# Performance work log

Measured on AMD Instinct MI355X. Metric: run time of the kernel, lower is better.

## Reference

```python
import jax, jax.numpy as jnp
import numpy as np

B, S1, S2, H, HM = 16, 128, 256, 256, 512  # batch, seq1, seq2, per-token hidden, mlp hidden


def setup_inputs() -> dict:
    k = jax.random.key(0)
    ks = jax.random.split(k, 7)
    query = jax.random.normal(ks[0], (B, S1, H), jnp.float32)
    key = jax.random.normal(ks[1], (B, S2, H), jnp.float32)
    value = jax.random.normal(ks[2], (B, S2, H), jnp.float32)
    q_mask = jax.random.randint(ks[3], (B, S1), 0, 2).astype(jnp.float32)
    k_mask = jax.random.randint(ks[4], (B, S2), 0, 2).astype(jnp.float32)
    s1 = 1.0 / np.sqrt(2 * H)
    W1 = jax.random.uniform(ks[5], (2 * H, HM), jnp.float32, -s1, s1)
    b1 = jnp.zeros((HM,), jnp.float32)
    s2 = 1.0 / np.sqrt(HM)
    W2 = jax.random.uniform(ks[6], (HM, 1), jnp.float32, -s2, s2)
    b2 = jnp.zeros((1,), jnp.float32)
    return {"query": query, "key": key, "value": value, "q_mask": q_mask,
            "k_mask": k_mask, "W1": W1, "b1": b1, "W2": W2, "b2": b2}


def reference(query, key, value, q_mask, k_mask, W1, b1, W2, b2):
    # Factor the first Linear over the concat: cat([q,k]) @ W1 == q @ W1[:H] + k @ W1[H:]
    Hq = query.shape[-1]
    qp = jnp.einsum('bqd,dh->bqh', query, W1[:Hq])      # [B,S1,HM]
    kp = jnp.einsum('bkd,dh->bkh', key, W1[Hq:])        # [B,S2,HM]
    hid = jax.nn.relu(qp[:, :, None, :] + kp[:, None, :, :] + b1)  # [B,S1,S2,HM]
    scores = jnp.einsum('bqkh,h->bqk', hid, W2[:, 0]) + b2[0]       # [B,S1,S2]
    mask = q_mask[:, :, None] * k_mask[:, None, :]                   # [B,S1,S2]
    # masked_fill(-inf).exp() == 0 at masked positions
    A = jnp.where(mask == 0, jnp.zeros((), scores.dtype), jnp.exp(scores))
    A_sum = jnp.clip(jnp.sum(A, axis=-1, keepdims=True), 2e-15, None)
    attn = A / A_sum
    return jnp.einsum('bqk,bkd->bqd', attn, value)  # [B,S1,H]
```

## Files before the change

kernel.cpp:

```cpp
#include <hip/hip_runtime.h>
#include <hip/hip_bf16.h>

#define B_  16
#define S1_ 128
#define S2_ 256
#define H_  256
#define HM_ 512
#define QB  4

typedef _Float16 hf2 __attribute__((ext_vector_type(2)));
typedef _Float16 hf4 __attribute__((ext_vector_type(4)));
typedef _Float16 hf8 __attribute__((ext_vector_type(8)));
typedef float    f32x4 __attribute__((ext_vector_type(4)));

static __device__ inline hf2 u2h(unsigned u) {
    union { unsigned u; hf2 h; } x; x.u = u; return x.h;
}

static __device__ inline float dot2(hf2 a, hf2 b, float c) {
#if __has_builtin(__builtin_amdgcn_fdot2)
    return __builtin_amdgcn_fdot2(a, b, c, false);
#else
    asm("v_dot2_f32_f16 %0, %1, %2, %0" : "+v"(c) : "v"(a), "v"(b));
    return c;
#endif
}

__global__ __launch_bounds__(256) void cvtWB_kernel(
    const float* __restrict__ W1, _Float16* __restrict__ WB)
{
    const int idx  = blockIdx.x * 256 + threadIdx.x;
    const int lane = idx & 63;
    const int nblk = (idx >> 6) & 31;
    const int kblk = idx >> 11;
    const int n    = nblk * 16 + (lane & 15);
    const int k0   = kblk * 32 + (lane >> 4) * 8;
    hf8 v;
#pragma unroll
    for (int j = 0; j < 8; ++j)
        v[j] = (_Float16)W1[(size_t)(k0 + j) * HM_ + n];
    *(hf8*)(WB + (size_t)idx * 8) = v;
}

#define ESTR 520

__global__ __launch_bounds__(512, 4) void proj_mfma_kernel(
    const float* __restrict__ query,
    const float* __restrict__ key,
    const _Float16* __restrict__ WB,
    const float* __restrict__ b1,
    _Float16* __restrict__ QPh,
    _Float16* __restrict__ KPTh)
{
    __shared__ _Float16 Es[16 * ESTR];

    const int t   = threadIdx.x;
    const int bid = blockIdx.x;
    const bool modeK = bid >= 128;
    const int m0  = (modeK ? bid - 128 : bid) * 16;
    const float* X = modeK ? key : query;
    const int kb  = modeK ? 8 : 0;

    {
        const int row = t >> 5, c8 = (t & 31) * 8;
        const float* xs = X + (size_t)(m0 + row) * H_ + c8;
        float4 xa = *(const float4*)xs;
        float4 xb = *(const float4*)(xs + 4);
        hf8 xh = { (_Float16)xa.x, (_Float16)xa.y, (_Float16)xa.z, (_Float16)xa.w,
                   (_Float16)xb.x, (_Float16)xb.y, (_Float16)xb.z, (_Float16)xb.w };
        *(hf8*)&Es[row * ESTR + c8] = xh;
    }
    __syncthreads();

    const int lane = t & 63, w = t >> 6;
    const int fr = lane & 15;
    const int fk = (lane >> 4) * 8;

    f32x4 acc[4] = {};

#pragma unroll
    for (int s = 0; s < 8; ++s) {
        hf8 a = *(const hf8*)&Es[fr * ESTR + s * 32 + fk];
        const _Float16* bp =
            WB + ((((size_t)(kb + s) * 32 + w * 4) * 64) + lane) * 8;
#pragma unroll
        for (int nf = 0; nf < 4; ++nf) {
            hf8 bv = *(const hf8*)(bp + (size_t)nf * 64 * 8);
            acc[nf] = __builtin_amdgcn_mfma_f32_16x16x32_f16(a, bv, acc[nf], 0, 0, 0);
        }
    }

    __syncthreads();

#pragma unroll
    for (int nf = 0; nf < 4; ++nf) {
        const int n = w * 64 + nf * 16 + fr;
        const float bv = modeK ? b1[n] : 0.f;
#pragma unroll
        for (int r = 0; r < 4; ++r) {
            const int ml = (lane >> 4) * 4 + r;
            Es[ml * ESTR + n] = (_Float16)(acc[nf][r] + bv);
        }
    }
    __syncthreads();

    if (!modeK) {
#pragma unroll
        for (int p = 0; p < 2; ++p) {
            const int idx = t + p * 512;
            const int row = idx >> 6, c8 = (idx & 63) * 8;
            *(uint4*)(QPh + (size_t)(m0 + row) * HM_ + c8) =
                *(const uint4*)&Es[row * ESTR + c8];
        }
    } else {
        const int bb = m0 >> 8, kbase = m0 & 255;
#pragma unroll
        for (int p = 0; p < 2; ++p) {
            const int idx = t + p * 512;
            const int h8 = idx >> 4, kl = idx & 15;
            *(uint4*)(KPTh + (((size_t)bb * 64 + h8) * 256 + kbase + kl) * 8) =
                *(const uint4*)&Es[kl * ESTR + h8 * 8];
        }
    }
}

__global__ __launch_bounds__(512, 4) void attn_kernel(
    const _Float16* __restrict__ QPh,
    const _Float16* __restrict__ KPTh,
    const float* __restrict__ value,
    const float* __restrict__ q_mask,
    const float* __restrict__ k_mask,
    const float* __restrict__ W2,
    const float* __restrict__ b2,
    float* __restrict__ out)
{
    __shared__ __align__(16) _Float16 qp_h[QB][HM_];
    __shared__ __align__(16) _Float16 w2_h[HM_];
    __shared__ __align__(16) float    Ap[2][QB][S2_];
    __shared__ __align__(16) float4   opart[8][QB][64];
    __shared__ float rA_s[QB];
    __shared__ float qm_s[QB];
    __shared__ float km_s[S2_];

    const int t  = threadIdx.x;
    const int k  = t & 255;
    const int hb = t >> 8;

    const int orig = blockIdx.x + (int)gridDim.x * blockIdx.y;
    const int wg   = (orig & 7) * 64 + (orig >> 3);
    const int q0   = (wg & 31) * QB;
    const int b    = wg >> 5;

    {
        if (t < 256) {
            const uint4* src = (const uint4*)(QPh + (size_t)(b * S1_ + q0) * HM_);
            ((uint4*)&qp_h[0][0])[t] = src[t];
            km_s[t] = k_mask[b * S2_ + t];
        } else if (t < 256 + 128) {
            const int i = t - 256;
            float4 wvv = ((const float4*)W2)[i];
            hf4 hv = { (_Float16)wvv.x, (_Float16)wvv.y,
                       (_Float16)wvv.z, (_Float16)wvv.w };
            *(hf4*)&w2_h[i * 4] = hv;
        } else if (t < 256 + 128 + QB) {
            const int i = t - (256 + 128);
            qm_s[i] = q_mask[b * S1_ + q0 + i];
        }
    }
    __syncthreads();

    float accs[QB] = {0.f, 0.f, 0.f, 0.f};
    const uint4* kp8 = (const uint4*)KPTh + ((size_t)b * 64 + hb * 32) * S2_ + k;

    for (int c = 0; c < 32; ++c) {
        uint4 kvu = kp8[(size_t)c * S2_];
        const int hoff = hb * (HM_ / 2) + c * 8;
        uint4 w4u = *(const uint4*)&w2_h[hoff];
        hf2 kv0 = u2h(kvu.x), kv1 = u2h(kvu.y), kv2 = u2h(kvu.z), kv3 = u2h(kvu.w);
        hf2 wv0 = u2h(w4u.x), wv1 = u2h(w4u.y), wv2 = u2h(w4u.z), wv3 = u2h(w4u.w);
        const hf2 zero = (hf2)(_Float16)0;
#pragma unroll
        for (int q = 0; q < QB; ++q) {
            uint4 qvu = *(const uint4*)&qp_h[q][hoff];
            hf2 s;
            s = __builtin_elementwise_max(u2h(qvu.x) + kv0, zero);
            accs[q] = dot2(s, wv0, accs[q]);
            s = __builtin_elementwise_max(u2h(qvu.y) + kv1, zero);
            accs[q] = dot2(s, wv1, accs[q]);
            s = __builtin_elementwise_max(u2h(qvu.z) + kv2, zero);
            accs[q] = dot2(s, wv2, accs[q]);
            s = __builtin_elementwise_max(u2h(qvu.w) + kv3, zero);
            accs[q] = dot2(s, wv3, accs[q]);
        }
    }
#pragma unroll
    for (int q = 0; q < QB; ++q) Ap[hb][q][k] = accs[q];
    __syncthreads();

    {
        const float b2v = b2[0];
#pragma unroll
        for (int i = 0; i < 2; ++i) {
            const int idx = t + i * 512;
            const int q = idx >> 8, kk = idx & 255;
            float sc = Ap[0][q][kk] + Ap[1][q][kk] + b2v;
            Ap[0][q][kk] = (qm_s[q] * km_s[kk] == 0.f) ? 0.f : __expf(sc);
        }
    }
    __syncthreads();

    if (t < QB * 64) {
        const int q = t >> 6, lane = t & 63;
        float p = Ap[0][q][lane] + Ap[0][q][lane + 64] +
                  Ap[0][q][lane + 128] + Ap[0][q][lane + 192];
#pragma unroll
        for (int m = 32; m >= 1; m >>= 1) p += __shfl_xor(p, m, 64);
        if (lane == 0) rA_s[q] = 1.0f / fmaxf(p, 2e-15f);
    }
    __syncthreads();

    {
        const int w = t >> 6, lane = t & 63;
        const float4* vb = (const float4*)(value + (size_t)b * S2_ * H_)
                           + (size_t)(w * 32) * (H_ / 4) + lane;
        float4 o[QB];
#pragma unroll
        for (int q = 0; q < QB; ++q) o[q] = make_float4(0.f, 0.f, 0.f, 0.f);
#pragma unroll 4
        for (int kk = 0; kk < 32; ++kk) {
            float4 v = vb[(size_t)kk * (H_ / 4)];
#pragma unroll
            for (int q = 0; q < QB; ++q) {
                float a = Ap[0][q][w * 32 + kk];
                o[q].x = fmaf(a, v.x, o[q].x); o[q].y = fmaf(a, v.y, o[q].y);
                o[q].z = fmaf(a, v.z, o[q].z); o[q].w = fmaf(a, v.w, o[q].w);
            }
        }
#pragma unroll
        for (int q = 0; q < QB; ++q) opart[w][q][lane] = o[q];
    }
    __syncthreads();

    if (t < QB * 64) {
        const int q = t >> 6, lane = t & 63;
        float4 s = make_float4(0.f, 0.f, 0.f, 0.f);
#pragma unroll
        for (int w = 0; w < 8; ++w) {
            float4 p = opart[w][q][lane];
            s.x += p.x; s.y += p.y; s.z += p.z; s.w += p.w;
        }
        const float r = rA_s[q];
        s.x *= r; s.y *= r; s.z *= r; s.w *= r;
        *(float4*)(out + (size_t)(b * S1_ + q0 + q) * H_ + lane * 4) = s;
    }
}

extern "C" void kernel_launch(void* const* d_in, const int* in_sizes, int n_in,
                              void* d_out, int out_size, void* d_ws, size_t ws_size,
                              hipStream_t stream) {
    const float* query  = (const float*)d_in[0];
    const float* key    = (const float*)d_in[1];
    const float* value  = (const float*)d_in[2];
    const float* q_mask = (const float*)d_in[3];
    const float* k_mask = (const float*)d_in[4];
    const float* W1     = (const float*)d_in[5];
    const float* b1     = (const float*)d_in[6];
    const float* W2     = (const float*)d_in[7];
    const float* b2     = (const float*)d_in[8];
    float*       out    = (float*)d_out;

    _Float16* QPh  = (_Float16*)d_ws;
    _Float16* KPTh = QPh  + (size_t)B_ * S1_ * HM_;
    _Float16* WB   = KPTh + (size_t)B_ * S2_ * HM_;

    cvtWB_kernel<<<128, 256, 0, stream>>>(W1, WB);

    proj_mfma_kernel<<<384, 512, 0, stream>>>(query, key, WB, b1, QPh, KPTh);

    attn_kernel<<<dim3(S1_ / QB, B_), 512, 0, stream>>>(
        QPh, KPTh, value, q_mask, k_mask, W2, b2, out);
}
```

Before: 40.13 us.

## Fuse three kernels into one cooperative kernel with grid-wide syncs

Result: slower. 146.4 us (+264.9%).

```diff
diff --git a/kernel.cpp b/kernel.cpp
--- a/kernel.cpp
+++ b/kernel.cpp
@@ -1,5 +1,8 @@
 #include <hip/hip_runtime.h>
 #include <hip/hip_bf16.h>
+#include <hip/hip_cooperative_groups.h>
+
+namespace cg = cooperative_groups;
 
 #define B_  16
 #define S1_ 128
@@ -7,6 +10,7 @@
 #define H_  256
 #define HM_ 512
 #define QB  4
+#define ESTR 520
 
 typedef _Float16 hf2 __attribute__((ext_vector_type(2)));
 typedef _Float16 hf4 __attribute__((ext_vector_type(4)));
@@ -26,232 +30,235 @@
 #endif
 }
 
-__global__ __launch_bounds__(256) void cvtWB_kernel(
-    const float* __restrict__ W1, _Float16* __restrict__ WB)
-{
-    const int idx  = blockIdx.x * 256 + threadIdx.x;
-    const int lane = idx & 63;
-    const int nblk = (idx >> 6) & 31;
-    const int kblk = idx >> 11;
-    const int n    = nblk * 16 + (lane & 15);
-    const int k0   = kblk * 32 + (lane >> 4) * 8;
-    hf8 v;
-#pragma unroll
-    for (int j = 0; j < 8; ++j)
-        v[j] = (_Float16)W1[(size_t)(k0 + j) * HM_ + n];
-    *(hf8*)(WB + (size_t)idx * 8) = v;
-}
-
-#define ESTR 520
-
-__global__ __launch_bounds__(512, 4) void proj_mfma_kernel(
+struct AttnS {
+    _Float16 qp_h[QB][HM_];
+    _Float16 w2_h[HM_];
+    float    Ap[2][QB][S2_];
+    float4   opart[8][QB][64];
+    float    rA_s[QB];
+    float    qm_s[QB];
+    float    km_s[S2_];
+};
+union SMemU {
+    AttnS    a;
+    _Float16 es[16 * ESTR];
+};
+
+__global__ __launch_bounds__(512, 4) void fused_kernel(
     const float* __restrict__ query,
     const float* __restrict__ key,
-    const _Float16* __restrict__ WB,
-    const float* __restrict__ b1,
-    _Float16* __restrict__ QPh,
-    _Float16* __restrict__ KPTh)
-{
-    __shared__ _Float16 Es[16 * ESTR];
-
-    const int t   = threadIdx.x;
-    const int bid = blockIdx.x;
-    const bool modeK = bid >= 128;
-    const int m0  = (modeK ? bid - 128 : bid) * 16;
-    const float* X = modeK ? key : query;
-    const int kb  = modeK ? 8 : 0;
-
-    {
-        const int row = t >> 5, c8 = (t & 31) * 8;
-        const float* xs = X + (size_t)(m0 + row) * H_ + c8;
-        float4 xa = *(const float4*)xs;
-        float4 xb = *(const float4*)(xs + 4);
-        hf8 xh = { (_Float16)xa.x, (_Float16)xa.y, (_Float16)xa.z, (_Float16)xa.w,
-                   (_Float16)xb.x, (_Float16)xb.y, (_Float16)xb.z, (_Float16)xb.w };
-        *(hf8*)&Es[row * ESTR + c8] = xh;
-    }
-    __syncthreads();
-
-    const int lane = t & 63, w = t >> 6;
-    const int fr = lane & 15;
-    const int fk = (lane >> 4) * 8;
-
-    f32x4 acc[4] = {};
-
-#pragma unroll
-    for (int s = 0; s < 8; ++s) {
-        hf8 a = *(const hf8*)&Es[fr * ESTR + s * 32 + fk];
-        const _Float16* bp =
-            WB + ((((size_t)(kb + s) * 32 + w * 4) * 64) + lane) * 8;
-#pragma unroll
-        for (int nf = 0; nf < 4; ++nf) {
-            hf8 bv = *(const hf8*)(bp + (size_t)nf * 64 * 8);
-            acc[nf] = __builtin_amdgcn_mfma_f32_16x16x32_f16(a, bv, acc[nf], 0, 0, 0);
-        }
-    }
-
-    __syncthreads();
-
-#pragma unroll
-    for (int nf = 0; nf < 4; ++nf) {
-        const int n = w * 64 + nf * 16 + fr;
-        const float bv = modeK ? b1[n] : 0.f;
-#pragma unroll
-        for (int r = 0; r < 4; ++r) {
-            const int ml = (lane >> 4) * 4 + r;
-            Es[ml * ESTR + n] = (_Float16)(acc[nf][r] + bv);
-        }
-    }
-    __syncthreads();
-
-    if (!modeK) {
-#pragma unroll
-        for (int p = 0; p < 2; ++p) {
-            const int idx = t + p * 512;
-            const int row = idx >> 6, c8 = (idx & 63) * 8;
-            *(uint4*)(QPh + (size_t)(m0 + row) * HM_ + c8) =
-                *(const uint4*)&Es[row * ESTR + c8];
-        }
-    } else {
-        const int bb = m0 >> 8, kbase = m0 & 255;
-#pragma unroll
-        for (int p = 0; p < 2; ++p) {
-            const int idx = t + p * 512;
-            const int h8 = idx >> 4, kl = idx & 15;
-            *(uint4*)(KPTh + (((size_t)bb * 64 + h8) * 256 + kbase + kl) * 8) =
-                *(const uint4*)&Es[kl * ESTR + h8 * 8];
-        }
-    }
-}
-
-__global__ __launch_bounds__(512, 4) void attn_kernel(
-    const _Float16* __restrict__ QPh,
-    const _Float16* __restrict__ KPTh,
     const float* __restrict__ value,
     const float* __restrict__ q_mask,
     const float* __restrict__ k_mask,
+    const float* __restrict__ W1,
+    const float* __restrict__ b1,
     const float* __restrict__ W2,
     const float* __restrict__ b2,
-    float* __restrict__ out)
+    float* __restrict__ out,
+    _Float16* __restrict__ QPh,
+    _Float16* __restrict__ KPTh,
+    _Float16* __restrict__ WB)
 {
-    __shared__ __align__(16) _Float16 qp_h[QB][HM_];
-    __shared__ __align__(16) _Float16 w2_h[HM_];
-    __shared__ __align__(16) float    Ap[2][QB][S2_];
-    __shared__ __align__(16) float4   opart[8][QB][64];
-    __shared__ float rA_s[QB];
-    __shared__ float qm_s[QB];
-    __shared__ float km_s[S2_];
-
-    const int t  = threadIdx.x;
-    const int k  = t & 255;
-    const int hb = t >> 8;
-
-    const int orig = blockIdx.x + (int)gridDim.x * blockIdx.y;
-    const int wg   = (orig & 7) * 64 + (orig >> 3);
-    const int q0   = (wg & 31) * QB;
-    const int b    = wg >> 5;
+    cg::grid_group grid = cg::this_grid();
+    __shared__ SMemU sm;
+
+    const int t   = threadIdx.x;
+    const int blk = blockIdx.x;
+
+    if (t < 64) {
+        const int idx  = blk * 64 + t;
+        const int lane = idx & 63;
+        const int nblk = (idx >> 6) & 31;
+        const int kblk = idx >> 11;
+        const int n    = nblk * 16 + (lane & 15);
+        const int k0   = kblk * 32 + (lane >> 4) * 8;
+        hf8 v;
+#pragma unroll
+        for (int j = 0; j < 8; ++j)
+            v[j] = (_Float16)W1[(size_t)(k0 + j) * HM_ + n];
+        *(hf8*)(WB + (size_t)idx * 8) = v;
+    }
+    grid.sync();
+
+    if (blk < 384) {
+        const bool modeK = blk >= 128;
+        const int m0  = (modeK ? blk - 128 : blk) * 16;
+        const float* X = modeK ? key : query;
+        const int kb  = modeK ? 8 : 0;
+
+        {
+            const int row = t >> 5, c8 = (t & 31) * 8;
+            const float* xs = X + (size_t)(m0 + row) * H_ + c8;
+            float4 xa = *(const float4*)xs;
+            float4 xb = *(const float4*)(xs + 4);
+            hf8 xh = { (_Float16)xa.x, (_Float16)xa.y, (_Float16)xa.z, (_Float16)xa.w,
+                       (_Float16)xb.x, (_Float16)xb.y, (_Float16)xb.z, (_Float16)xb.w };
+            *(hf8*)&sm.es[row * ESTR + c8] = xh;
+        }
+        __syncthreads();
+
+        const int lane = t & 63, w = t >> 6;
+        const int fr = lane & 15;
+        const int fk = (lane >> 4) * 8;
+
+        f32x4 acc[4] = {};
+#pragma unroll
+        for (int s = 0; s < 8; ++s) {
+            hf8 a = *(const hf8*)&sm.es[fr * ESTR + s * 32 + fk];
+            const _Float16* bp =
+                WB + ((((size_t)(kb + s) * 32 + w * 4) * 64) + lane) * 8;
+#pragma unroll
+            for (int nf = 0; nf < 4; ++nf) {
+                hf8 bv = *(const hf8*)(bp + (size_t)nf * 64 * 8);
+                acc[nf] = __builtin_amdgcn_mfma_f32_16x16x32_f16(a, bv, acc[nf], 0, 0, 0);
+            }
+        }
+
+        __syncthreads();
+
+#pragma unroll
+        for (int nf = 0; nf < 4; ++nf) {
+            const int n = w * 64 + nf * 16 + fr;
+            const float bv = modeK ? b1[n] : 0.f;
+#pragma unroll
+            for (int r = 0; r < 4; ++r) {
+                const int ml = (lane >> 4) * 4 + r;
+                sm.es[ml * ESTR + n] = (_Float16)(acc[nf][r] + bv);
+            }
+        }
+        __syncthreads();
+
+        if (!modeK) {
+#pragma unroll
+            for (int p = 0; p < 2; ++p) {
+                const int idx = t + p * 512;
+                const int row = idx >> 6, c8 = (idx & 63) * 8;
+                *(uint4*)(QPh + (size_t)(m0 + row) * HM_ + c8) =
+                    *(const uint4*)&sm.es[row * ESTR + c8];
+            }
+        } else {
+            const int bb = m0 >> 8, kbase = m0 & 255;
+#pragma unroll
+            for (int p = 0; p < 2; ++p) {
+                const int idx = t + p * 512;
+                const int h8 = idx >> 4, kl = idx & 15;
+                *(uint4*)(KPTh + (((size_t)bb * 64 + h8) * 256 + kbase + kl) * 8) =
+                    *(const uint4*)&sm.es[kl * ESTR + h8 * 8];
+            }
+        }
+    }
+    grid.sync();
 
     {
+        const int k  = t & 255;
+        const int hb = t >> 8;
+
+        const int orig = blk;
+        const int wg   = (orig & 7) * 64 + (orig >> 3);
+        const int q0   = (wg & 31) * QB;
+        const int b    = wg >> 5;
+
         if (t < 256) {
             const uint4* src = (const uint4*)(QPh + (size_t)(b * S1_ + q0) * HM_);
-            ((uint4*)&qp_h[0][0])[t] = src[t];
-            km_s[t] = k_mask[b * S2_ + t];
+            ((uint4*)&sm.a.qp_h[0][0])[t] = src[t];
+            sm.a.km_s[t] = k_mask[b * S2_ + t];
         } else if (t < 256 + 128) {
             const int i = t - 256;
             float4 wvv = ((const float4*)W2)[i];
             hf4 hv = { (_Float16)wvv.x, (_Float16)wvv.y,
                        (_Float16)wvv.z, (_Float16)wvv.w };
-            *(hf4*)&w2_h[i * 4] = hv;
+            *(hf4*)&sm.a.w2_h[i * 4] = hv;
         } else if (t < 256 + 128 + QB) {
             const int i = t - (256 + 128);
-            qm_s[i] = q_mask[b * S1_ + q0 + i];
-        }
-    }
-    __syncthreads();
-
-    float accs[QB] = {0.f, 0.f, 0.f, 0.f};
-    const uint4* kp8 = (const uint4*)KPTh + ((size_t)b * 64 + hb * 32) * S2_ + k;
-
-    for (int c = 0; c < 32; ++c) {
-        uint4 kvu = kp8[(size_t)c * S2_];
-        const int hoff = hb * (HM_ / 2) + c * 8;
-        uint4 w4u = *(const uint4*)&w2_h[hoff];
-        hf2 kv0 = u2h(kvu.x), kv1 = u2h(kvu.y), kv2 = u2h(kvu.z), kv3 = u2h(kvu.w);
-        hf2 wv0 = u2h(w4u.x), wv1 = u2h(w4u.y), wv2 = u2h(w4u.z), wv3 = u2h(w4u.w);
-        const hf2 zero = (hf2)(_Float16)0;
-#pragma unroll
-        for (int q = 0; q < QB; ++q) {
-            uint4 qvu = *(const uint4*)&qp_h[q][hoff];
-            hf2 s;
-            s = __builtin_elementwise_max(u2h(qvu.x) + kv0, zero);
-            accs[q] = dot2(s, wv0, accs[q]);
-            s = __builtin_elementwise_max(u2h(qvu.y) + kv1, zero);
-            accs[q] = dot2(s, wv1, accs[q]);
-            s = __builtin_elementwise_max(u2h(qvu.z) + kv2, zero);
-            accs[q] = dot2(s, wv2, accs[q]);
-            s = __builtin_elementwise_max(u2h(qvu.w) + kv3, zero);
-            accs[q] = dot2(s, wv3, accs[q]);
-        }
-    }
-#pragma unroll
-    for (int q = 0; q < QB; ++q) Ap[hb][q][k] = accs[q];
-    __syncthreads();
-
-    {
-        const float b2v = b2[0];
-#pragma unroll
-        for (int i = 0; i < 2; ++i) {
-            const int idx = t + i * 512;
-            const int q = idx >> 8, kk = idx & 255;
-            float sc = Ap[0][q][kk] + Ap[1][q][kk] + b2v;
-            Ap[0][q][kk] = (qm_s[q] * km_s[kk] == 0.f) ? 0.f : __expf(sc);
-        }
-    }
-    __syncthreads();
-
-    if (t < QB * 64) {
-        const int q = t >> 6, lane = t & 63;
-        float p = Ap[0][q][lane] + Ap[0][q][lane + 64] +
-                  Ap[0][q][lane + 128] + Ap[0][q][lane + 192];
-#pragma unroll
-        for (int m = 32; m >= 1; m >>= 1) p += __shfl_xor(p, m, 64);
-        if (lane == 0) rA_s[q] = 1.0f / fmaxf(p, 2e-15f);
-    }
-    __syncthreads();
-
-    {
-        const int w = t >> 6, lane = t & 63;
-        const float4* vb = (const float4*)(value + (size_t)b * S2_ * H_)
-                           + (size_t)(w * 32) * (H_ / 4) + lane;
-        float4 o[QB];
-#pragma unroll
-        for (int q = 0; q < QB; ++q) o[q] = make_float4(0.f, 0.f, 0.f, 0.f);
+            sm.a.qm_s[i] = q_mask[b * S1_ + q0 + i];
+        }
+        __syncthreads();
+
+        float accs[QB] = {0.f, 0.f, 0.f, 0.f};
+        const uint4* kp8 = (const uint4*)KPTh + ((size_t)b * 64 + hb * 32) * S2_ + k;
+
+        for (int c = 0; c < 32; ++c) {
+            uint4 kvu = kp8[(size_t)c * S2_];
+            const int hoff = hb * (HM_ / 2) + c * 8;
+            uint4 w4u = *(const uint4*)&sm.a.w2_h[hoff];
+            hf2 kv0 = u2h(kvu.x), kv1 = u2h(kvu.y), kv2 = u2h(kvu.z), kv3 = u2h(kvu.w);
+            hf2 wv0 = u2h(w4u.x), wv1 = u2h(w4u.y), wv2 = u2h(w4u.z), wv3 = u2h(w4u.w);
+            const hf2 zero = (hf2)(_Float16)0;
+#pragma unroll
+            for (int q = 0; q < QB; ++q) {
+                uint4 qvu = *(const uint4*)&sm.a.qp_h[q][hoff];
+                hf2 s;
+                s = __builtin_elementwise_max(u2h(qvu.x) + kv0, zero);
+                accs[q] = dot2(s, wv0, accs[q]);
+                s = __builtin_elementwise_max(u2h(qvu.y) + kv1, zero);
+                accs[q] = dot2(s, wv1, accs[q]);
+                s = __builtin_elementwise_max(u2h(qvu.z) + kv2, zero);
+                accs[q] = dot2(s, wv2, accs[q]);
+                s = __builtin_elementwise_max(u2h(qvu.w) + kv3, zero);
+                accs[q] = dot2(s, wv3, accs[q]);
+            }
+        }
+#pragma unroll
+        for (int q = 0; q < QB; ++q) sm.a.Ap[hb][q][k] = accs[q];
+        __syncthreads();
+
+        {
+            const float b2v = b2[0];
+#pragma unroll
+            for (int i = 0; i < 2; ++i) {
+                const int idx = t + i * 512;
+                const int q = idx >> 8, kk = idx & 255;
+                float sc = sm.a.Ap[0][q][kk] + sm.a.Ap[1][q][kk] + b2v;
+                sm.a.Ap[0][q][kk] =
+                    (sm.a.qm_s[q] * sm.a.km_s[kk] == 0.f) ? 0.f : __expf(sc);
+            }
+        }
+        __syncthreads();
+
+        if (t < QB * 64) {
+            const int q = t >> 6, lane = t & 63;
+            float p = sm.a.Ap[0][q][lane] + sm.a.Ap[0][q][lane + 64] +
+                      sm.a.Ap[0][q][lane + 128] + sm.a.Ap[0][q][lane + 192];
+#pragma unroll
+            for (int m = 32; m >= 1; m >>= 1) p += __shfl_xor(p, m, 64);
+            if (lane == 0) sm.a.rA_s[q] = 1.0f / fmaxf(p, 2e-15f);
+        }
+        __syncthreads();
+
+        {
+            const int w = t >> 6, lane = t & 63;
+            const float4* vb = (const float4*)(value + (size_t)b * S2_ * H_)
+                               + (size_t)(w * 32) * (H_ / 4) + lane;
+            float4 o[QB];
+#pragma unroll
+            for (int q = 0; q < QB; ++q) o[q] = make_float4(0.f, 0.f, 0.f, 0.f);
 #pragma unroll 4
-        for (int kk = 0; kk < 32; ++kk) {
-            float4 v = vb[(size_t)kk * (H_ / 4)];
-#pragma unroll
-            for (int q = 0; q < QB; ++q) {
-                float a = Ap[0][q][w * 32 + kk];
-                o[q].x = fmaf(a, v.x, o[q].x); o[q].y = fmaf(a, v.y, o[q].y);
-                o[q].z = fmaf(a, v.z, o[q].z); o[q].w = fmaf(a, v.w, o[q].w);
-            }
-        }
-#pragma unroll
-        for (int q = 0; q < QB; ++q) opart[w][q][lane] = o[q];
-    }
-    __syncthreads();
-
-    if (t < QB * 64) {
-        const int q = t >> 6, lane = t & 63;
-        float4 s = make_float4(0.f, 0.f, 0.f, 0.f);
-#pragma unroll
-        for (int w = 0; w < 8; ++w) {
-            float4 p = opart[w][q][lane];
-            s.x += p.x; s.y += p.y; s.z += p.z; s.w += p.w;
-        }
-        const float r = rA_s[q];
-        s.x *= r; s.y *= r; s.z *= r; s.w *= r;
-        *(float4*)(out + (size_t)(b * S1_ + q0 + q) * H_ + lane * 4) = s;
+            for (int kk = 0; kk < 32; ++kk) {
+                float4 v = vb[(size_t)kk * (H_ / 4)];
+#pragma unroll
+                for (int q = 0; q < QB; ++q) {
+                    float a = sm.a.Ap[0][q][w * 32 + kk];
+                    o[q].x = fmaf(a, v.x, o[q].x); o[q].y = fmaf(a, v.y, o[q].y);
+                    o[q].z = fmaf(a, v.z, o[q].z); o[q].w = fmaf(a, v.w, o[q].w);
+                }
+            }
+#pragma unroll
+            for (int q = 0; q < QB; ++q) sm.a.opart[w][q][lane] = o[q];
+        }
+        __syncthreads();
+
+        if (t < QB * 64) {
+            const int q = t >> 6, lane = t & 63;
+            float4 s = make_float4(0.f, 0.f, 0.f, 0.f);
+#pragma unroll
+            for (int w = 0; w < 8; ++w) {
+                float4 p = sm.a.opart[w][q][lane];
+                s.x += p.x; s.y += p.y; s.z += p.z; s.w += p.w;
+            }
+            const float r = sm.a.rA_s[q];
+            s.x *= r; s.y *= r; s.z *= r; s.w *= r;
+            *(float4*)(out + (size_t)(b * S1_ + q0 + q) * H_ + lane * 4) = s;
+        }
     }
 }
 
@@ -273,10 +280,12 @@
     _Float16* KPTh = QPh  + (size_t)B_ * S1_ * HM_;
     _Float16* WB   = KPTh + (size_t)B_ * S2_ * HM_;
 
-    cvtWB_kernel<<<128, 256, 0, stream>>>(W1, WB);
-
-    proj_mfma_kernel<<<384, 512, 0, stream>>>(query, key, WB, b1, QPh, KPTh);
-
-    attn_kernel<<<dim3(S1_ / QB, B_), 512, 0, stream>>>(
-        QPh, KPTh, value, q_mask, k_mask, W2, b2, out);
-}
+    void* args[] = {
+        (void*)&query, (void*)&key, (void*)&value,
+        (void*)&q_mask, (void*)&k_mask,
+        (void*)&W1, (void*)&b1, (void*)&W2, (void*)&b2,
+        (void*)&out, (void*)&QPh, (void*)&KPTh, (void*)&WB
+    };
+    hipLaunchCooperativeKernel((void*)fused_kernel, dim3(512), dim3(512),
+                               args, 0, stream);
+}
```
